# Kernel tuning notes

Hardware: AMD Instinct MI355X
Metric: run time of the kernel (lower is better)

## Reference

```python
import jax, jax.numpy as jnp
import numpy as np

B, N, L = 16, 512, 512          # batch, compound atoms, protein words
DIM = 10                         # compound feature dim
DM, H, DK, DFF = 128, 8, 16, 512 # transformer dims
LG, LO = 3, 3                    # layer_gnn, layer_output
NFP, NW = 10000, 10000           # vocab sizes
NEG = -9e15                      # GAT mask sentinel (matches torch code)


def _layernorm(x, g, b, eps=1e-6):
    # annotated-transformer LayerNorm: unbiased std, eps added to std
    m = jnp.mean(x, -1, keepdims=True)
    s = jnp.std(x, -1, keepdims=True, ddof=1)
    return g * (x - m) / (s + eps) + b


def _pos_encoding(length, d_model):
    pos = np.arange(length)[:, None]
    div = np.exp(np.arange(0, d_model, 2) * (-np.log(10000.0) / d_model))
    pe = np.zeros((length, d_model), np.float32)
    pe[:, 0::2] = np.sin(pos * div)
    pe[:, 1::2] = np.cos(pos * div)
    return jnp.asarray(pe)


def setup_inputs():
    ks = iter(jax.random.split(jax.random.key(0), 64))
    def nrm(shape, scale):
        return jax.random.normal(next(ks), shape, jnp.float32) * scale
    return dict(
        fingerprints=jax.random.randint(next(ks), (B, N), 0, NFP, jnp.int32),
        fp_mask=jnp.ones((B, N), jnp.float32),
        adjacency=jax.random.randint(next(ks), (B, N, N), 0, 2, jnp.int32),
        words=jax.random.randint(next(ks), (B, L), 0, NW, jnp.int32),
        words_mask=jnp.ones((B, L), jnp.float32),
        emb_fp=nrm((NFP, DIM), 0.1),
        emb_word=nrm((NW, DM), 0.1),
        Wg=nrm((LG, DIM, DIM), 0.3), bg=jnp.zeros((LG, DIM), jnp.float32),
        attn_a=nrm((LG, 2 * DIM), 0.3),
        Wq=nrm((DM, DM), 0.09), bq=jnp.zeros((DM,), jnp.float32),
        Wk=nrm((DM, DM), 0.09), bk=jnp.zeros((DM,), jnp.float32),
        Wv=nrm((DM, DM), 0.09), bv=jnp.zeros((DM,), jnp.float32),
        Wo=nrm((DM, DM), 0.09), bo=jnp.zeros((DM,), jnp.float32),
        ln1_g=jnp.ones((DM,), jnp.float32), ln1_b=jnp.zeros((DM,), jnp.float32),
        ln2_g=jnp.ones((DM,), jnp.float32), ln2_b=jnp.zeros((DM,), jnp.float32),
        lnf_g=jnp.ones((DM,), jnp.float32), lnf_b=jnp.zeros((DM,), jnp.float32),
        W1=nrm((DM, DFF), 0.09), b1=jnp.zeros((DFF,), jnp.float32),
        W2=nrm((DFF, DM), 0.045), b2=jnp.zeros((DM,), jnp.float32),
        Wtout=nrm((DM, DIM), 0.09), btout=jnp.zeros((DIM,), jnp.float32),
        Watt=nrm((DIM, DIM), 0.3), batt=jnp.zeros((DIM,), jnp.float32),
        Wout=nrm((LO, 2 * DIM, 2 * DIM), 0.2), bout=jnp.zeros((LO, 2 * DIM), jnp.float32),
        Wint=nrm((2 * DIM, 2), 0.2), bint=jnp.zeros((2,), jnp.float32),
    )


def _forward(fingerprints, fp_mask, adjacency, words, words_mask,
             emb_fp, emb_word, Wg, bg, attn_a,
             Wq, bq, Wk, bk, Wv, bv, Wo, bo,
             ln1_g, ln1_b, ln2_g, ln2_b, lnf_g, lnf_b,
             W1, b1, W2, b2, Wtout, btout,
             Watt, batt, Wout, bout, Wint, bint):
    # ---- GAT over compound graph (dropout disabled = eval/deterministic) ----
    xs = emb_fp[fingerprints]                     # [B,N,DIM]
    mask = fp_mask[:, :, None]                    # [B,N,1]
    adj = adjacency > 0
    for i in range(LG):
        h = jax.nn.relu(xs @ Wg[i] + bg[i]) * mask
        # e[b,i,j] = leaky_relu(a1.h_i + a2.h_j)  == leaky_relu([h_i||h_j] @ a)
        s1 = h @ attn_a[i, :DIM]                  # [B,N]
        s2 = h @ attn_a[i, DIM:]                  # [B,N]
        e = jax.nn.leaky_relu(s1[:, :, None] + s2[:, None, :])  # [B,N,N]
        att = jax.nn.softmax(jnp.where(adj, e, NEG), axis=2)
        xs = xs + att @ h
    compound = jnp.mean(xs * mask, axis=1, keepdims=True)       # [B,1,DIM]

    # ---- transformer encoder, 1 layer, annotated-transformer (pre-norm) ----
    x = emb_word[words] * jnp.sqrt(jnp.float32(DM)) + _pos_encoding(L, DM)
    m4 = words_mask[:, None, None, :] > 0         # [B,1,1,L]
    xn = _layernorm(x, ln1_g, ln1_b)
    heads = lambda t: t.reshape(B, L, H, DK).transpose(0, 2, 1, 3)
    q, k, v = heads(xn @ Wq + bq), heads(xn @ Wk + bk), heads(xn @ Wv + bv)
    scores = jnp.einsum('bhqd,bhkd->bhqk', q, k) / jnp.sqrt(jnp.float32(DK))
    p = jax.nn.softmax(jnp.where(m4, scores, -1e9), axis=-1)
    attn = jnp.einsum('bhqk,bhkd->bhqd', p, v).transpose(0, 2, 1, 3).reshape(B, L, DM)
    x = x + (attn @ Wo + bo)
    xn = _layernorm(x, ln2_g, ln2_b)
    x = x + (jax.nn.relu(xn @ W1 + b1) @ W2 + b2)
    x = _layernorm(x, lnf_g, lnf_b)
    word_vectors = jax.nn.relu(x) @ Wtout + btout  # [B,L,DIM]

    # ---- tanh cross-attention (attention_cnn) ----
    hc = jax.nn.relu(compound @ Watt + batt)       # [B,1,DIM]
    hp = jax.nn.relu(word_vectors @ Watt + batt)   # [B,L,DIM]
    w = jnp.tanh(jnp.einsum('bxd,bld->bxl', hc, hp))  # [B,1,L]
    protein = jnp.mean(w.transpose(0, 2, 1) * hp, axis=1, keepdims=True)  # [B,1,DIM]

    cat = jnp.concatenate([compound, protein], axis=2)  # [B,1,2*DIM]
    for j in range(LO):
        cat = jax.nn.relu(cat @ Wout[j] + bout[j])
    return jnp.squeeze(cat @ Wint + bint, axis=1)        # [B,2]


def reference(fingerprints, fp_mask, adjacency, words, words_mask,
              emb_fp, emb_word, Wg, bg, attn_a,
              Wq, bq, Wk, bk, Wv, bv, Wo, bo,
              ln1_g, ln1_b, ln2_g, ln2_b, lnf_g, lnf_b,
              W1, b1, W2, b2, Wtout, btout,
              Watt, batt, Wout, bout, Wint, bint):
    return _forward(fingerprints, fp_mask, adjacency, words, words_mask,
                    emb_fp, emb_word, Wg, bg, attn_a,
                    Wq, bq, Wk, bk, Wv, bv, Wo, bo,
                    ln1_g, ln1_b, ln2_g, ln2_b, lnf_g, lnf_b,
                    W1, b1, W2, b2, Wtout, btout,
                    Watt, batt, Wout, bout, Wint, bint)
```

## Files before the change

kernel.cpp:

```cpp
#include <hip/hip_runtime.h>
#include <hip/hip_bf16.h>
#include <math.h>

#define B 16
#define N 512
#define L 512
#define DIM 10
#define DM 128
#define H 8
#define DK 16
#define DFF 512
#define LG 3
#define LO 3
#define NEGV -9.0e15f
#define RF 16
#define AQR 64
#define KSEG 256
#define RLOG2E 1.44269504f

__device__ __forceinline__ float wave_reduce_sum(float v) {
    #pragma unroll
    for (int o = 32; o > 0; o >>= 1) v += __shfl_down(v, o, 64);
    return v;
}

__device__ __forceinline__ float quad_sum(float x) {
    int y1 = __builtin_amdgcn_mov_dpp(__float_as_int(x), 0xB1, 0xF, 0xF, true);
    float s = x + __int_as_float(y1);
    int y2 = __builtin_amdgcn_mov_dpp(__float_as_int(s), 0x4E, 0xF, 0xF, true);
    return s + __int_as_float(y2);
}

__device__ __forceinline__ float half_reduce_sum(float v) {
    #pragma unroll
    for (int o = 16; o > 0; o >>= 1) v += __shfl_xor(v, o, 64);
    return v;
}

__device__ __forceinline__ float fast_exp2(float x) {
    return __builtin_amdgcn_exp2f(x);
}


__global__ void k_gnn_h(const int* __restrict__ fing, const float* __restrict__ emb_fp,
                        float* __restrict__ xs, const float* __restrict__ fp_mask,
                        const float* __restrict__ Wg, const float* __restrict__ bg,
                        const float* __restrict__ aatt,
                        float* __restrict__ h, float* __restrict__ s1, float* __restrict__ s2,
                        int first) {
    int bn = blockIdx.x * blockDim.x + threadIdx.x;
    if (bn >= B * N) return;
    float x[DIM];
    if (first) {
        long base = (long)fing[bn] * DIM;
        #pragma unroll
        for (int d = 0; d < DIM; d++) { x[d] = emb_fp[base + d]; xs[bn * DIM + d] = x[d]; }
    } else {
        #pragma unroll
        for (int d = 0; d < DIM; d++) x[d] = xs[bn * DIM + d];
    }
    float m = fp_mask[bn];
    float a1 = 0.f, a2 = 0.f;
    #pragma unroll
    for (int j = 0; j < DIM; j++) {
        float acc = bg[j];
        #pragma unroll
        for (int d = 0; d < DIM; d++) acc += x[d] * Wg[d * DIM + j];
        acc = fmaxf(acc, 0.f) * m;
        h[bn * DIM + j] = acc;
        a1 += acc * aatt[j];
        a2 += acc * aatt[DIM + j];
    }
    s1[bn] = a1;
    s2[bn] = a2;
}

__global__ void k_gnn_att(const float* __restrict__ h, const float* __restrict__ s1,
                          const float* __restrict__ s2, const int* __restrict__ adj,
                          float* __restrict__ xs) {
    int b  = blockIdx.x / (N / 16);
    int rg = blockIdx.x % (N / 16);
    int t = threadIdx.x;
    int g  = t >> 4;
    int ll = t & 15;
    int i = rg * 16 + g;

    __shared__ float h_s[N * DIM];
    __shared__ float s2_s[N];

    const float* hb = h + (long)b * N * DIM;
    for (int idx = t; idx < N * DIM; idx += 256) h_s[idx] = hb[idx];
    for (int j = t; j < N; j += 256) s2_s[j] = s2[b * N + j];
    __syncthreads();

    float s1v = s1[b * N + i];
    const int* adjrow = adj + ((long)b * N + i) * N;

    float sum = 0.f;
    float a[DIM];
    #pragma unroll
    for (int d = 0; d < DIM; d++) a[d] = 0.f;
    #pragma unroll
    for (int c = 0; c < 32; c++) {
        int j = c * 16 + ll;
        float xsc = s1v + s2_s[j];
        xsc = xsc > 0.f ? xsc : 0.01f * xsc;
        float e = (adjrow[j] > 0) ? xsc : NEGV;
        float p = fast_exp2(e * RLOG2E);
        sum += p;
        #pragma unroll
        for (int d = 0; d < DIM; d++) a[d] += p * h_s[j * DIM + d];
    }
    #pragma unroll
    for (int off = 1; off < 16; off <<= 1) {
        sum += __shfl_xor(sum, off, 64);
        #pragma unroll
        for (int d = 0; d < DIM; d++) a[d] += __shfl_xor(a[d], off, 64);
    }
    if (ll < DIM) {
        float av = a[0];
        if (ll == 1) av = a[1]; else if (ll == 2) av = a[2]; else if (ll == 3) av = a[3];
        else if (ll == 4) av = a[4]; else if (ll == 5) av = a[5]; else if (ll == 6) av = a[6];
        else if (ll == 7) av = a[7]; else if (ll == 8) av = a[8]; else if (ll == 9) av = a[9];
        xs[((long)b * N + i) * DIM + ll] += av / sum;
    }
}

__global__ void k_compound(const float* __restrict__ xs, const float* __restrict__ fp_mask,
                           const float* __restrict__ Watt, const float* __restrict__ batt,
                           float* __restrict__ compound, float* __restrict__ hc) {
    int b = blockIdx.x;
    int t = threadIdx.x;
    int wid = t >> 6, lane = t & 63;
    float lacc[DIM];
    #pragma unroll
    for (int d = 0; d < DIM; d++) lacc[d] = 0.f;
    for (int n = t; n < N; n += 256) {
        float m = fp_mask[b * N + n];
        #pragma unroll
        for (int d = 0; d < DIM; d++) lacc[d] += xs[((long)b * N + n) * DIM + d] * m;
    }
    __shared__ float red[4][DIM];
    __shared__ float comp_s[DIM];
    #pragma unroll
    for (int d = 0; d < DIM; d++) lacc[d] = wave_reduce_sum(lacc[d]);
    if (lane == 0) {
        #pragma unroll
        for (int d = 0; d < DIM; d++) red[wid][d] = lacc[d];
    }
    __syncthreads();
    if (t < DIM) {
        float c = (red[0][t] + red[1][t] + red[2][t] + red[3][t]) / (float)N;
        compound[b * DIM + t] = c;
        comp_s[t] = c;
    }
    __syncthreads();
    if (t < DIM) {
        float acc = batt[t];
        #pragma unroll
        for (int e = 0; e < DIM; e++) acc += comp_s[e] * Watt[e * DIM + t];
        hc[b * DIM + t] = fmaxf(acc, 0.f);
    }
}


__global__ void k_embed_ln(const int* __restrict__ words, const float* __restrict__ emb,
                           const float* __restrict__ g, const float* __restrict__ bb,
                           float* __restrict__ x, float* __restrict__ xn) {
    int row = blockIdx.x;
    int t = threadIdx.x;
    int wid = t >> 6, lane = t & 63;
    int l = row % L;
    int k2 = (t >> 1) * 2;
    double div = exp((double)k2 * (-log(10000.0) / (double)DM));
    double ang = (double)l * div;
    float pev = (t & 1) ? (float)cos(ang) : (float)sin(ang);
    float v = emb[(long)words[row] * DM + t] * sqrtf(128.0f) + pev;
    x[(long)row * DM + t] = v;
    float s = wave_reduce_sum(v);
    __shared__ float r2[2], r3[2];
    if (lane == 0) r2[wid] = s;
    __syncthreads();
    float mean = (r2[0] + r2[1]) / (float)DM;
    float dv = v - mean;
    float q = wave_reduce_sum(dv * dv);
    if (lane == 0) r3[wid] = q;
    __syncthreads();
    float sd = sqrtf((r3[0] + r3[1]) / (float)(DM - 1)) + 1e-6f;
    xn[(long)row * DM + t] = g[t] * dv / sd + bb[t];
}

__global__ void k_qkv(const float* __restrict__ xn,
                      const float* __restrict__ Wq, const float* __restrict__ bq,
                      const float* __restrict__ Wk, const float* __restrict__ bk,
                      const float* __restrict__ Wv, const float* __restrict__ bv,
                      float* __restrict__ q, float* __restrict__ k, float* __restrict__ v) {
    long row0 = (long)blockIdx.x * RF;
    int t = threadIdx.x;
    __shared__ float xs_s[RF * DM];
    for (int i = t; i < RF * DM; i += 384) xs_s[i] = xn[row0 * DM + i];
    __syncthreads();
    int proj = t / DM;
    int j = t % DM;
    const float* W    = proj == 0 ? Wq : (proj == 1 ? Wk : Wv);
    const float* bias = proj == 0 ? bq : (proj == 1 ? bk : bv);
    float* out        = proj == 0 ? q  : (proj == 1 ? k  : v);
    float acc[RF];
    #pragma unroll
    for (int r = 0; r < RF; r++) acc[r] = bias[j];
    for (int d4 = 0; d4 < DM / 4; d4++) {
        float w0 = W[(4 * d4 + 0) * DM + j];
        float w1 = W[(4 * d4 + 1) * DM + j];
        float w2 = W[(4 * d4 + 2) * DM + j];
        float w3 = W[(4 * d4 + 3) * DM + j];
        #pragma unroll
        for (int r = 0; r < RF; r++) {
            float4 xv = ((const float4*)&xs_s[r * DM])[d4];
            acc[r] += xv.x * w0 + xv.y * w1 + xv.z * w2 + xv.w * w3;
        }
    }
    #pragma unroll
    for (int r = 0; r < RF; r++) {
        long row = row0 + r;
        int b = (int)(row / L), l = (int)(row % L);
        out[(((long)b * H + j / DK) * L + l) * DK + (j % DK)] = acc[r];
    }
}

__global__ void __launch_bounds__(256, 4)
k_attn(const float* __restrict__ q, const float* __restrict__ k,
       const float* __restrict__ v, const float* __restrict__ wmask,
       float* __restrict__ attn_p, float* __restrict__ ssum_p) {
    int blk = blockIdx.x;
    int seg = blk & 1;
    int rest = blk >> 1;
    int qc = rest % (L / AQR);
    int bh = rest / (L / AQR);
    int b = bh / H, hh = bh % H;
    int t = threadIdx.x;
    int sl = t & 3;
    int r = t >> 2;
    int l = qc * AQR + r;
    int j00 = seg * KSEG;

    __shared__ float4 k_s[KSEG * 4];
    __shared__ float wm_s[KSEG];
    const float4* kb4 = (const float4*)(k + (long)bh * L * DK) + (long)j00 * 4;
    for (int i = t; i < KSEG * 4; i += 256) k_s[i] = kb4[i];
    for (int j = t; j < KSEG; j += 256)
        wm_s[j] = (wmask[b * L + j00 + j] > 0.f) ? 0.f : -1.443e9f;
    __syncthreads();

    float4 qr = ((const float4*)(q + ((long)bh * L + l) * DK))[sl];
    const float qsc = 0.25f * RLOG2E;
    qr.x *= qsc; qr.y *= qsc; qr.z *= qsc; qr.w *= qsc;

    const float4* vb4 = (const float4*)(v + (long)bh * L * DK) + (long)j00 * 4;

    float ssum = 0.f;
    float4 acc = make_float4(0.f, 0.f, 0.f, 0.f);

    for (int c = 0; c < KSEG / 8; c++) {
        int j0 = c * 8;
        float s8[8];
        #pragma unroll
        for (int jj = 0; jj < 8; jj++) {
            float4 kk = k_s[(j0 + jj) * 4 + sl];
            float part = qr.x * kk.x + qr.y * kk.y + qr.z * kk.z + qr.w * kk.w;
            s8[jj] = quad_sum(part);
        }
        const float4* mp = (const float4*)&wm_s[j0];
        float4 ma = mp[0], mb = mp[1];
        s8[0] += ma.x; s8[1] += ma.y; s8[2] += ma.z; s8[3] += ma.w;
        s8[4] += mb.x; s8[5] += mb.y; s8[6] += mb.z; s8[7] += mb.w;

        #pragma unroll
        for (int jj = 0; jj < 8; jj++) {
            float p = fast_exp2(s8[jj]);
            ssum += p;
            float4 vv = vb4[(j0 + jj) * 4 + sl];
            acc.x += p * vv.x; acc.y += p * vv.y; acc.z += p * vv.z; acc.w += p * vv.w;
        }
    }

    float4* outp = (float4*)(attn_p + (((long)seg * B + b) * L + l) * DM + hh * DK);
    outp[sl] = acc;
    if (sl == 0) ssum_p[(((long)seg * B + b) * H + hh) * L + l] = ssum;
}

__global__ void k_oproj(const float* __restrict__ attn_p, const float* __restrict__ ssum_p,
                        const float* __restrict__ Wo, const float* __restrict__ bo,
                        float* __restrict__ x) {
    long row0 = (long)blockIdx.x * RF;
    int t = threadIdx.x;
    int b = (int)(row0 / L);
    int l0 = (int)(row0 % L);

    __shared__ float a_s[RF * DM];
    __shared__ float inv_s[RF][H];

    {
        int row = t >> 3, hh = t & 7;
        float s0 = ssum_p[(((long)0 * B + b) * H + hh) * L + (l0 + row)];
        float s1 = ssum_p[(((long)1 * B + b) * H + hh) * L + (l0 + row)];
        inv_s[row][hh] = 1.f / (s0 + s1);
    }
    __syncthreads();

    const float4* p0 = (const float4*)(attn_p + (((long)0 * B + b) * L + l0) * DM);
    const float4* p1 = (const float4*)(attn_p + (((long)1 * B + b) * L + l0) * DM);
    for (int i = t; i < RF * DM / 4; i += 128) {
        float4 a0 = p0[i], a1 = p1[i];
        int row = i >> 5;
        int hh = (i & 31) >> 2;
        float inv = inv_s[row][hh];
        ((float4*)a_s)[i] = make_float4((a0.x + a1.x) * inv, (a0.y + a1.y) * inv,
                                        (a0.z + a1.z) * inv, (a0.w + a1.w) * inv);
    }
    __syncthreads();

    float acc[RF];
    #pragma unroll
    for (int r = 0; r < RF; r++) acc[r] = bo[t];
    for (int d4 = 0; d4 < DM / 4; d4++) {
        float w0 = Wo[(4 * d4 + 0) * DM + t];
        float w1 = Wo[(4 * d4 + 1) * DM + t];
        float w2 = Wo[(4 * d4 + 2) * DM + t];
        float w3 = Wo[(4 * d4 + 3) * DM + t];
        #pragma unroll
        for (int r = 0; r < RF; r++) {
            float4 av = ((const float4*)&a_s[r * DM])[d4];
            acc[r] += av.x * w0 + av.y * w1 + av.z * w2 + av.w * w3;
        }
    }
    #pragma unroll
    for (int r = 0; r < RF; r++) x[(row0 + r) * DM + t] += acc[r];
}

__global__ void k_ffn_fused(const float* __restrict__ x,
                            const float* __restrict__ ln2_g, const float* __restrict__ ln2_b,
                            const float* __restrict__ W1, const float* __restrict__ b1,
                            const float* __restrict__ W2, const float* __restrict__ b2,
                            const float* __restrict__ lnf_g, const float* __restrict__ lnf_b,
                            const float* __restrict__ Wtout, const float* __restrict__ btout,
                            const float* __restrict__ Watt, const float* __restrict__ batt,
                            float* __restrict__ hp) {
    long row0 = (long)blockIdx.x * RF;
    int t = threadIdx.x;

    __shared__ float x_s[RF][DM];
    __shared__ float xn_s[RF][DM];
    __shared__ float h_s[RF][DFF];
    __shared__ float r_s[RF][DM + 4];
    __shared__ float wt_s[DM * DIM];
    __shared__ float wa_s[DIM * DIM];
    __shared__ float bt_s[DIM], ba_s[DIM];
    __shared__ float wv_s[RF][DIM];

    {
        float4 xv = ((const float4*)(x + row0 * DM))[t];
        ((float4*)&x_s[0][0])[t] = xv;
        for (int i = t; i < DM * DIM; i += 512) wt_s[i] = Wtout[i];
        for (int i = t; i < DIM * DIM; i += 512) wa_s[i] = Watt[i];
        if (t < DIM) { bt_s[t] = btout[t]; ba_s[t] = batt[t]; }
    }
    __syncthreads();

    {
        int row = t >> 5, c = t & 31;
        float4 v = ((const float4*)&x_s[row][0])[c];
        float s = half_reduce_sum(v.x + v.y + v.z + v.w);
        float mean = s / (float)DM;
        float4 dv = make_float4(v.x - mean, v.y - mean, v.z - mean, v.w - mean);
        float q = half_reduce_sum(dv.x * dv.x + dv.y * dv.y + dv.z * dv.z + dv.w * dv.w);
        float sd = sqrtf(q / (float)(DM - 1)) + 1e-6f;
        const float4 g4 = ((const float4*)ln2_g)[c];
        const float4 b4 = ((const float4*)ln2_b)[c];
        ((float4*)&xn_s[row][0])[c] = make_float4(
            g4.x * dv.x / sd + b4.x, g4.y * dv.y / sd + b4.y,
            g4.z * dv.z / sd + b4.z, g4.w * dv.w / sd + b4.w);
    }
    __syncthreads();

    {
        float acc[RF];
        #pragma unroll
        for (int r = 0; r < RF; r++) acc[r] = b1[t];
        for (int d4 = 0; d4 < DM / 4; d4++) {
            float w0 = W1[(4 * d4 + 0) * DFF + t];
            float w1 = W1[(4 * d4 + 1) * DFF + t];
            float w2 = W1[(4 * d4 + 2) * DFF + t];
            float w3 = W1[(4 * d4 + 3) * DFF + t];
            #pragma unroll
            for (int r = 0; r < RF; r++) {
                float4 xv = ((const float4*)&xn_s[r][0])[d4];
                acc[r] += xv.x * w0 + xv.y * w1 + xv.z * w2 + xv.w * w3;
            }
        }
        #pragma unroll
        for (int r = 0; r < RF; r++) h_s[r][t] = fmaxf(acc[r], 0.f);
    }
    __syncthreads();

    {
        int col = t & 127, rq = t >> 7;
        float acc2[4];
        #pragma unroll
        for (int rr = 0; rr < 4; rr++) acc2[rr] = b2[col];
        for (int f4 = 0; f4 < DFF / 4; f4++) {
            float w0 = W2[(4 * f4 + 0) * DM + col];
            float w1 = W2[(4 * f4 + 1) * DM + col];
            float w2 = W2[(4 * f4 + 2) * DM + col];
            float w3 = W2[(4 * f4 + 3) * DM + col];
            #pragma unroll
            for (int rr = 0; rr < 4; rr++) {
                float4 hv = ((const float4*)&h_s[rq * 4 + rr][0])[f4];
                acc2[rr] += hv.x * w0 + hv.y * w1 + hv.z * w2 + hv.w * w3;
            }
        }
        __syncthreads();
        #pragma unroll
        for (int rr = 0; rr < 4; rr++) {
            int row = rq * 4 + rr;
            xn_s[row][col] = x_s[row][col] + acc2[rr];
        }
    }
    __syncthreads();

    {
        int row = t >> 5, c = t & 31;
        float4 v = ((const float4*)&xn_s[row][0])[c];
        float s = half_reduce_sum(v.x + v.y + v.z + v.w);
        float mean = s / (float)DM;
        float4 dv = make_float4(v.x - mean, v.y - mean, v.z - mean, v.w - mean);
        float q = half_reduce_sum(dv.x * dv.x + dv.y * dv.y + dv.z * dv.z + dv.w * dv.w);
        float sd = sqrtf(q / (float)(DM - 1)) + 1e-6f;
        const float4 g4 = ((const float4*)lnf_g)[c];
        const float4 b4 = ((const float4*)lnf_b)[c];
        r_s[row][4 * c + 0] = fmaxf(g4.x * dv.x / sd + b4.x, 0.f);
        r_s[row][4 * c + 1] = fmaxf(g4.y * dv.y / sd + b4.y, 0.f);
        r_s[row][4 * c + 2] = fmaxf(g4.z * dv.z / sd + b4.z, 0.f);
        r_s[row][4 * c + 3] = fmaxf(g4.w * dv.w / sd + b4.w, 0.f);
    }
    __syncthreads();

    if (t < RF * DIM) {
        int row = t / DIM, o = t % DIM;
        float acc = bt_s[o];
        for (int d = 0; d < DM; d++) acc += r_s[row][d] * wt_s[d * DIM + o];
        wv_s[row][o] = acc;
    }
    __syncthreads();

    if (t < RF * DIM) {
        int row = t / DIM, o = t % DIM;
        float acc = ba_s[o];
        #pragma unroll
        for (int e = 0; e < DIM; e++) acc += wv_s[row][e] * wa_s[e * DIM + o];
        hp[(row0 + row) * DIM + o] = fmaxf(acc, 0.f);
    }
}

__global__ void k_final(const float* __restrict__ hp, const float* __restrict__ hc,
                        const float* __restrict__ compound, const float* __restrict__ Wout,
                        const float* __restrict__ bout, const float* __restrict__ Wint,
                        const float* __restrict__ bint, float* __restrict__ out) {
    int b = blockIdx.x;
    int t = threadIdx.x;
    int wid = t >> 6, lane = t & 63;

    __shared__ float wout_s[LO * 2 * DIM * 2 * DIM];
    __shared__ float bout_s[LO * 2 * DIM];
    __shared__ float wint_s[2 * DIM * 2];
    __shared__ float bint_s[2];
    __shared__ float hc_s[DIM];
    __shared__ float red[4][DIM];
    __shared__ float cat_s[2 * DIM];
    __shared__ float tmp_s[2 * DIM];

    for (int i = t; i < LO * 2 * DIM * 2 * DIM; i += 256) wout_s[i] = Wout[i];
    for (int i = t; i < LO * 2 * DIM; i += 256) bout_s[i] = bout[i];
    for (int i = t; i < 2 * DIM * 2; i += 256) wint_s[i] = Wint[i];
    if (t < 2) bint_s[t] = bint[t];
    if (t < DIM) hc_s[t] = hc[b * DIM + t];
    __syncthreads();

    float lacc[DIM];
    #pragma unroll
    for (int e = 0; e < DIM; e++) lacc[e] = 0.f;
    for (int l = t; l < L; l += 256) {
        const float* hpl = hp + ((long)b * L + l) * DIM;
        float hv[DIM];
        float dot = 0.f;
        #pragma unroll
        for (int e = 0; e < DIM; e++) { hv[e] = hpl[e]; dot += hc_s[e] * hv[e]; }
        float w = tanhf(dot);
        #pragma unroll
        for (int e = 0; e < DIM; e++) lacc[e] += w * hv[e];
    }
    #pragma unroll
    for (int e = 0; e < DIM; e++) lacc[e] = wave_reduce_sum(lacc[e]);
    if (lane == 0) {
        #pragma unroll
        for (int e = 0; e < DIM; e++) red[wid][e] = lacc[e];
    }
    __syncthreads();
    if (t < DIM) {
        cat_s[t] = compound[b * DIM + t];
        cat_s[DIM + t] = (red[0][t] + red[1][t] + red[2][t] + red[3][t]) / (float)L;
    }
    __syncthreads();

    for (int j = 0; j < LO; j++) {
        float acc = 0.f;
        if (t < 2 * DIM) {
            acc = bout_s[j * 2 * DIM + t];
            #pragma unroll
            for (int e = 0; e < 2 * DIM; e++)
                acc += cat_s[e] * wout_s[j * 2 * DIM * 2 * DIM + e * 2 * DIM + t];
            acc = fmaxf(acc, 0.f);
            tmp_s[t] = acc;
        }
        __syncthreads();
        if (t < 2 * DIM) cat_s[t] = tmp_s[t];
        __syncthreads();
    }
    if (t < 2) {
        float o = bint_s[t];
        #pragma unroll
        for (int e = 0; e < 2 * DIM; e++) o += cat_s[e] * wint_s[e * 2 + t];
        out[b * 2 + t] = o;
    }
}

extern "C" void kernel_launch(void* const* d_in, const int* in_sizes, int n_in,
                              void* d_out, int out_size, void* d_ws, size_t ws_size,
                              hipStream_t stream) {
    (void)in_sizes; (void)n_in; (void)out_size; (void)ws_size;
    const int*   fingerprints = (const int*)d_in[0];
    const float* fp_mask      = (const float*)d_in[1];
    const int*   adjacency    = (const int*)d_in[2];
    const int*   words        = (const int*)d_in[3];
    const float* words_mask   = (const float*)d_in[4];
    const float* emb_fp       = (const float*)d_in[5];
    const float* emb_word     = (const float*)d_in[6];
    const float* Wg   = (const float*)d_in[7];
    const float* bg   = (const float*)d_in[8];
    const float* attn_a = (const float*)d_in[9];
    const float* Wq = (const float*)d_in[10];
    const float* bq = (const float*)d_in[11];
    const float* Wk = (const float*)d_in[12];
    const float* bk = (const float*)d_in[13];
    const float* Wv = (const float*)d_in[14];
    const float* bv = (const float*)d_in[15];
    const float* Wo = (const float*)d_in[16];
    const float* bo = (const float*)d_in[17];
    const float* ln1_g = (const float*)d_in[18];
    const float* ln1_b = (const float*)d_in[19];
    const float* ln2_g = (const float*)d_in[20];
    const float* ln2_b = (const float*)d_in[21];
    const float* lnf_g = (const float*)d_in[22];
    const float* lnf_b = (const float*)d_in[23];
    const float* W1 = (const float*)d_in[24];
    const float* b1 = (const float*)d_in[25];
    const float* W2 = (const float*)d_in[26];
    const float* b2 = (const float*)d_in[27];
    const float* Wtout = (const float*)d_in[28];
    const float* btout = (const float*)d_in[29];
    const float* Watt  = (const float*)d_in[30];
    const float* batt  = (const float*)d_in[31];
    const float* Wout  = (const float*)d_in[32];
    const float* bout  = (const float*)d_in[33];
    const float* Wint  = (const float*)d_in[34];
    const float* bint  = (const float*)d_in[35];
    float* out = (float*)d_out;

    float* w = (float*)d_ws;
    float* xs = w;        w += B * N * DIM;
    float* h  = w;        w += B * N * DIM;
    float* s1 = w;        w += B * N;
    float* s2 = w;        w += B * N;
    float* compound = w;  w += B * DIM;
    float* hc = w;        w += B * DIM;
    float* x  = w;        w += (long)B * L * DM;
    float* xn = w;        w += (long)B * L * DM;
    float* qb = w;        w += (long)B * H * L * DK;
    float* kb = w;        w += (long)B * H * L * DK;
    float* vb = w;        w += (long)B * H * L * DK;
    float* attn_p = w;    w += 2L * B * L * DM;
    float* ssum_p = w;    w += 2L * B * H * L;
    float* hp = w;        w += (long)B * L * DIM;

    for (int i = 0; i < LG; i++) {
        k_gnn_h<<<(B * N + 255) / 256, 256, 0, stream>>>(
            fingerprints, emb_fp, xs, fp_mask,
            Wg + i * DIM * DIM, bg + i * DIM, attn_a + i * 2 * DIM, h, s1, s2, i == 0);
        k_gnn_att<<<B * (N / 16), 256, 0, stream>>>(h, s1, s2, adjacency, xs);
    }
    k_compound<<<B, 256, 0, stream>>>(xs, fp_mask, Watt, batt, compound, hc);

    k_embed_ln<<<B * L, DM, 0, stream>>>(words, emb_word, ln1_g, ln1_b, x, xn);
    k_qkv<<<B * L / RF, 3 * DM, 0, stream>>>(xn, Wq, bq, Wk, bk, Wv, bv, qb, kb, vb);
    k_attn<<<B * H * (L / AQR) * 2, 256, 0, stream>>>(qb, kb, vb, words_mask, attn_p, ssum_p);
    k_oproj<<<B * L / RF, DM, 0, stream>>>(attn_p, ssum_p, Wo, bo, x);
    k_ffn_fused<<<B * L / RF, DFF, 0, stream>>>(x, ln2_g, ln2_b, W1, b1, W2, b2,
                                                lnf_g, lnf_b, Wtout, btout, Watt, batt, hp);
    k_final<<<B, 256, 0, stream>>>(hp, hc, compound, Wout, bout, Wint, bint, out);
}
```

Measured before the change: 232.3 us.

## Rework attention split to 2 lanes per query, 4 key segments; pad GAT smem

The attention kernel now assigns two lanes per query row, each handling 8 head dims, so each block covers 128 queries. Keys are split into four segments of 128 instead of two of 256, and the output projection sums four partial results. This cuts shuffle reductions per score and reuses each K/V load across more queries, at the cost of larger partial buffers and more reduction traffic. In the GAT attention, node features and s2 are packed into 12-float padded rows read with float4, and the log2e scaling is folded into s1/s2 at write time.

```diff
diff --git a/kernel.cpp b/kernel.cpp
--- a/kernel.cpp
+++ b/kernel.cpp
@@ -14,8 +14,9 @@
 #define LO 3
 #define NEGV -9.0e15f
 #define RF 16
-#define AQR 64
-#define KSEG 256
+#define AQR2 128
+#define KSEG 128
+#define NSEG (L / KSEG)
 #define RLOG2E 1.44269504f
 
 __device__ __forceinline__ float wave_reduce_sum(float v) {
@@ -24,11 +25,9 @@
     return v;
 }
 
-__device__ __forceinline__ float quad_sum(float x) {
-    int y1 = __builtin_amdgcn_mov_dpp(__float_as_int(x), 0xB1, 0xF, 0xF, true);
-    float s = x + __int_as_float(y1);
-    int y2 = __builtin_amdgcn_mov_dpp(__float_as_int(s), 0x4E, 0xF, 0xF, true);
-    return s + __int_as_float(y2);
+__device__ __forceinline__ float pair_sum(float x) {
+    int y = __builtin_amdgcn_mov_dpp(__float_as_int(x), 0xB1, 0xF, 0xF, true);
+    return x + __int_as_float(y);
 }
 
 __device__ __forceinline__ float half_reduce_sum(float v) {
@@ -71,8 +70,8 @@
         a1 += acc * aatt[j];
         a2 += acc * aatt[DIM + j];
     }
-    s1[bn] = a1;
-    s2[bn] = a2;
+    s1[bn] = a1 * RLOG2E;
+    s2[bn] = a2 * RLOG2E;
 }
 
 __global__ void k_gnn_att(const float* __restrict__ h, const float* __restrict__ s1,
@@ -85,12 +84,17 @@
     int ll = t & 15;
     int i = rg * 16 + g;
 
-    __shared__ float h_s[N * DIM];
-    __shared__ float s2_s[N];
+    __shared__ float h_s[N * 12];
 
     const float* hb = h + (long)b * N * DIM;
-    for (int idx = t; idx < N * DIM; idx += 256) h_s[idx] = hb[idx];
-    for (int j = t; j < N; j += 256) s2_s[j] = s2[b * N + j];
+    for (int idx = t; idx < N * DIM; idx += 256) {
+        int node = idx / DIM, d = idx - node * DIM;
+        h_s[node * 12 + d] = hb[idx];
+    }
+    for (int j = t; j < N; j += 256) {
+        h_s[j * 12 + 10] = s2[b * N + j];
+        h_s[j * 12 + 11] = 0.f;
+    }
     __syncthreads();
 
     float s1v = s1[b * N + i];
@@ -103,13 +107,16 @@
     #pragma unroll
     for (int c = 0; c < 32; c++) {
         int j = c * 16 + ll;
-        float xsc = s1v + s2_s[j];
+        const float4* hp4 = (const float4*)&h_s[j * 12];
+        float4 h0 = hp4[0], h1 = hp4[1], h2 = hp4[2];
+        float xsc = s1v + h2.z;
         xsc = xsc > 0.f ? xsc : 0.01f * xsc;
         float e = (adjrow[j] > 0) ? xsc : NEGV;
-        float p = fast_exp2(e * RLOG2E);
+        float p = fast_exp2(e);
         sum += p;
-        #pragma unroll
-        for (int d = 0; d < DIM; d++) a[d] += p * h_s[j * DIM + d];
+        a[0] += p * h0.x; a[1] += p * h0.y; a[2] += p * h0.z; a[3] += p * h0.w;
+        a[4] += p * h1.x; a[5] += p * h1.y; a[6] += p * h1.z; a[7] += p * h1.w;
+        a[8] += p * h2.x; a[9] += p * h2.y;
     }
     #pragma unroll
     for (int off = 1; off < 16; off <<= 1) {
@@ -232,15 +239,15 @@
        const float* __restrict__ v, const float* __restrict__ wmask,
        float* __restrict__ attn_p, float* __restrict__ ssum_p) {
     int blk = blockIdx.x;
-    int seg = blk & 1;
-    int rest = blk >> 1;
-    int qc = rest % (L / AQR);
-    int bh = rest / (L / AQR);
+    int seg = blk & (NSEG - 1);
+    int rest = blk >> 2;
+    int qc = rest % (L / AQR2);
+    int bh = rest / (L / AQR2);
     int b = bh / H, hh = bh % H;
     int t = threadIdx.x;
-    int sl = t & 3;
-    int r = t >> 2;
-    int l = qc * AQR + r;
+    int sl = t & 1;
+    int r = t >> 1;
+    int l = qc * AQR2 + r;
     int j00 = seg * KSEG;
 
     __shared__ float4 k_s[KSEG * 4];
@@ -251,23 +258,27 @@
         wm_s[j] = (wmask[b * L + j00 + j] > 0.f) ? 0.f : -1.443e9f;
     __syncthreads();
 
-    float4 qr = ((const float4*)(q + ((long)bh * L + l) * DK))[sl];
+    const float4* qp = (const float4*)(q + ((long)bh * L + l) * DK);
+    float4 qa = qp[sl * 2], qb = qp[sl * 2 + 1];
     const float qsc = 0.25f * RLOG2E;
-    qr.x *= qsc; qr.y *= qsc; qr.z *= qsc; qr.w *= qsc;
+    qa.x *= qsc; qa.y *= qsc; qa.z *= qsc; qa.w *= qsc;
+    qb.x *= qsc; qb.y *= qsc; qb.z *= qsc; qb.w *= qsc;
 
     const float4* vb4 = (const float4*)(v + (long)bh * L * DK) + (long)j00 * 4;
 
     float ssum = 0.f;
-    float4 acc = make_float4(0.f, 0.f, 0.f, 0.f);
+    float4 a0 = make_float4(0.f, 0.f, 0.f, 0.f), a1 = a0;
 
     for (int c = 0; c < KSEG / 8; c++) {
         int j0 = c * 8;
         float s8[8];
         #pragma unroll
         for (int jj = 0; jj < 8; jj++) {
-            float4 kk = k_s[(j0 + jj) * 4 + sl];
-            float part = qr.x * kk.x + qr.y * kk.y + qr.z * kk.z + qr.w * kk.w;
-            s8[jj] = quad_sum(part);
+            float4 ka = k_s[(j0 + jj) * 4 + sl * 2];
+            float4 kb_ = k_s[(j0 + jj) * 4 + sl * 2 + 1];
+            float part = qa.x * ka.x + qa.y * ka.y + qa.z * ka.z + qa.w * ka.w
+                       + qb.x * kb_.x + qb.y * kb_.y + qb.z * kb_.z + qb.w * kb_.w;
+            s8[jj] = pair_sum(part);
         }
         const float4* mp = (const float4*)&wm_s[j0];
         float4 ma = mp[0], mb = mp[1];
@@ -278,13 +289,16 @@
         for (int jj = 0; jj < 8; jj++) {
             float p = fast_exp2(s8[jj]);
             ssum += p;
-            float4 vv = vb4[(j0 + jj) * 4 + sl];
-            acc.x += p * vv.x; acc.y += p * vv.y; acc.z += p * vv.z; acc.w += p * vv.w;
+            float4 va  = vb4[(j0 + jj) * 4 + sl * 2];
+            float4 vb2 = vb4[(j0 + jj) * 4 + sl * 2 + 1];
+            a0.x += p * va.x;  a0.y += p * va.y;  a0.z += p * va.z;  a0.w += p * va.w;
+            a1.x += p * vb2.x; a1.y += p * vb2.y; a1.z += p * vb2.z; a1.w += p * vb2.w;
         }
     }
 
     float4* outp = (float4*)(attn_p + (((long)seg * B + b) * L + l) * DM + hh * DK);
-    outp[sl] = acc;
+    outp[sl * 2]     = a0;
+    outp[sl * 2 + 1] = a1;
     if (sl == 0) ssum_p[(((long)seg * B + b) * H + hh) * L + l] = ssum;
 }
 
@@ -301,21 +315,27 @@
 
     {
         int row = t >> 3, hh = t & 7;
-        float s0 = ssum_p[(((long)0 * B + b) * H + hh) * L + (l0 + row)];
-        float s1 = ssum_p[(((long)1 * B + b) * H + hh) * L + (l0 + row)];
-        inv_s[row][hh] = 1.f / (s0 + s1);
+        float s = 0.f;
+        #pragma unroll
+        for (int sg = 0; sg < NSEG; sg++)
+            s += ssum_p[(((long)sg * B + b) * H + hh) * L + (l0 + row)];
+        inv_s[row][hh] = 1.f / s;
     }
     __syncthreads();
 
     const float4* p0 = (const float4*)(attn_p + (((long)0 * B + b) * L + l0) * DM);
     const float4* p1 = (const float4*)(attn_p + (((long)1 * B + b) * L + l0) * DM);
+    const float4* p2 = (const float4*)(attn_p + (((long)2 * B + b) * L + l0) * DM);
+    const float4* p3 = (const float4*)(attn_p + (((long)3 * B + b) * L + l0) * DM);
     for (int i = t; i < RF * DM / 4; i += 128) {
-        float4 a0 = p0[i], a1 = p1[i];
+        float4 a0 = p0[i], a1 = p1[i], a2 = p2[i], a3 = p3[i];
         int row = i >> 5;
         int hh = (i & 31) >> 2;
         float inv = inv_s[row][hh];
-        ((float4*)a_s)[i] = make_float4((a0.x + a1.x) * inv, (a0.y + a1.y) * inv,
-                                        (a0.z + a1.z) * inv, (a0.w + a1.w) * inv);
+        ((float4*)a_s)[i] = make_float4((a0.x + a1.x + a2.x + a3.x) * inv,
+                                        (a0.y + a1.y + a2.y + a3.y) * inv,
+                                        (a0.z + a1.z + a2.z + a3.z) * inv,
+                                        (a0.w + a1.w + a2.w + a3.w) * inv);
     }
     __syncthreads();
 
@@ -587,8 +607,8 @@
     float* qb = w;        w += (long)B * H * L * DK;
     float* kb = w;        w += (long)B * H * L * DK;
     float* vb = w;        w += (long)B * H * L * DK;
-    float* attn_p = w;    w += 2L * B * L * DM;
-    float* ssum_p = w;    w += 2L * B * H * L;
+    float* attn_p = w;    w += (long)NSEG * B * L * DM;
+    float* ssum_p = w;    w += (long)NSEG * B * H * L;
     float* hp = w;        w += (long)B * L * DIM;
 
     for (int i = 0; i < LG; i++) {
@@ -601,7 +621,7 @@
 
     k_embed_ln<<<B * L, DM, 0, stream>>>(words, emb_word, ln1_g, ln1_b, x, xn);
     k_qkv<<<B * L / RF, 3 * DM, 0, stream>>>(xn, Wq, bq, Wk, bk, Wv, bv, qb, kb, vb);
-    k_attn<<<B * H * (L / AQR) * 2, 256, 0, stream>>>(qb, kb, vb, words_mask, attn_p, ssum_p);
+    k_attn<<<B * H * (L / AQR2) * NSEG, 256, 0, stream>>>(qb, kb, vb, words_mask, attn_p, ssum_p);
     k_oproj<<<B * L / RF, DM, 0, stream>>>(attn_p, ssum_p, Wo, bo, x);
     k_ffn_fused<<<B * L / RF, DFF, 0, stream>>>(x, ln2_g, ln2_b, W1, b1, W2, b2,
                                                 lnf_g, lnf_b, Wtout, btout, Watt, batt, hp);
```

Measured after the change: 225.9 us. 1.03x faster.
